# Kernel optimization log

Measured on AMD Instinct MI355X. Metric: run time of the kernel, lower is better.

Reference implementation:

```python
import jax, jax.numpy as jnp
import numpy as np

EPS = 1e-5

def _ln_stats(x):
    mu = jnp.mean(x, axis=-1, keepdims=True)
    var = jnp.mean((x - mu) ** 2, axis=-1, keepdims=True)
    return (x - mu) * jax.lax.rsqrt(var + EPS)

def setup_inputs() -> dict:
    B, S, H, I, E = 2, 2048, 1024, 4096, 8
    key = jax.random.key(0)
    ks = jax.random.split(key, 8)
    inp = {
        "hidden_states": jax.random.normal(ks[0], (B, S, H), dtype=jnp.float32),
        "router_ln_w": jnp.ones((H,), jnp.float32),
        "router_ln_b": jnp.zeros((H,), jnp.float32),
        "router_w": jax.random.normal(ks[1], (H, E), dtype=jnp.float32) * 0.02,
        "router_b": jnp.zeros((E,), jnp.float32),
        "exp_ln_w": jnp.ones((E, H), jnp.float32),
        "exp_ln_b": jnp.zeros((E, H), jnp.float32),
        "w1": jax.random.normal(ks[2], (E, H, I), dtype=jnp.float32) * 0.02,
        "b1": jnp.zeros((E, I), jnp.float32),
        "w2": jax.random.normal(ks[3], (E, I, H), dtype=jnp.float32) * 0.02,
        "b2": jnp.zeros((E, H), jnp.float32),
        "out_ln_w": jnp.ones((H,), jnp.float32),
        "out_ln_b": jnp.zeros((H,), jnp.float32),
    }
    return inp

def reference(hidden_states, router_ln_w, router_ln_b, router_w, router_b,
              exp_ln_w, exp_ln_b, w1, b1, w2, b2, out_ln_w, out_ln_b):
    K = 2  # experts_per_token
    x = hidden_states  # [B,S,H]
    xhat = _ln_stats(x)  # normalized (pre-affine) stats shared across LNs on x

    # Router: LayerNorm -> Linear -> top-k -> softmax over the k logits
    router_logits = (xhat * router_ln_w + router_ln_b) @ router_w + router_b  # [B,S,E]
    routing_weights, selected = jax.lax.top_k(router_logits, K)  # [B,S,K]
    routing_weights = jax.nn.softmax(routing_weights, axis=-1)

    # Dense per-expert pass over ALL tokens (faithful to the original),
    # dropout is identity in eval mode.
    xn = xhat[None] * exp_ln_w[:, None, None, :] + exp_ln_b[:, None, None, :]  # [E,B,S,H]
    h = jnp.einsum('ebsh,ehi->ebsi', xn, w1) + b1[:, None, None, :]            # [E,B,S,I]
    h = jax.nn.gelu(h, approximate=False)
    eo = jnp.einsum('ebsi,eih->ebsh', h, w2) + b2[:, None, None, :]            # [E,B,S,H]

    # Masked combine == gather selected experts and weight-sum (top-k indices are distinct)
    eo = jnp.moveaxis(eo, 0, 2)  # [B,S,E,H]
    gathered = jnp.take_along_axis(eo, selected[..., None], axis=2)  # [B,S,K,H]
    combined = jnp.sum(routing_weights[..., None] * gathered, axis=2)  # [B,S,H]

    return _ln_stats(combined) * out_ln_w + out_ln_b
```

## Files before the change

kernel.cpp:

```cpp
#include <hip/hip_runtime.h>
#include <hip/hip_bf16.h>

#define T_TOK 4096
#define HDIM 1024
#define IDIM 4096
#define NEXP 8

typedef __bf16 bf16x8 __attribute__((ext_vector_type(8)));
typedef float f32x4 __attribute__((ext_vector_type(4)));
typedef unsigned short us8 __attribute__((ext_vector_type(8)));

__device__ __forceinline__ unsigned short f2bf(float f) {
    union { float f; unsigned int u; } v; v.f = f;
    unsigned int u = v.u;
    unsigned int r = u + 0x7fffu + ((u >> 16) & 1u);
    return (unsigned short)(r >> 16);
}
__device__ __forceinline__ float bf2f(unsigned short b) {
    union { unsigned int u; float f; } v; v.u = ((unsigned int)b) << 16;
    return v.f;
}

__device__ __forceinline__ void gll16(const unsigned short* g, unsigned short* lds) {
    __builtin_amdgcn_global_load_lds(
        (const __attribute__((address_space(1))) unsigned int*)g,
        (__attribute__((address_space(3))) unsigned int*)lds, 16, 0, 0);
}

__device__ __forceinline__ float gelu_f(float v) {
    float x = v * 0.70710678118654752f;
    float ax = fabsf(x);
    float t = __builtin_amdgcn_rcpf(1.0f + 0.3275911f * ax);
    float p = t * (0.254829592f + t * (-0.284496736f + t * (1.421413741f
              + t * (-1.453152027f + t * 1.061405429f))));
    float ex = __expf(-x * x);
    float er = 1.0f - p * ex;
    er = copysignf(er, x);
    return 0.5f * v * (1.0f + er);
}

__global__ __launch_bounds__(256) void k_cvt_t(const float* __restrict__ src,
                                               unsigned short* __restrict__ dst,
                                               int R, int C) {
    __shared__ unsigned short tl[64][72];
    const int e = blockIdx.z;
    const int c0 = blockIdx.x * 64, r0 = blockIdx.y * 64;
    const int tid = threadIdx.x;
    #pragma unroll
    for (int it = 0; it < 4; it++) {
        int idx = it * 256 + tid;
        int rl = idx >> 4, cl = (idx & 15) * 4;
        float4 v = *(const float4*)(src + ((size_t)e * R + r0 + rl) * C + c0 + cl);
        tl[cl + 0][rl] = f2bf(v.x);
        tl[cl + 1][rl] = f2bf(v.y);
        tl[cl + 2][rl] = f2bf(v.z);
        tl[cl + 3][rl] = f2bf(v.w);
    }
    __syncthreads();
    #pragma unroll
    for (int it = 0; it < 2; it++) {
        int idx = it * 256 + tid;
        int cl = idx >> 3, ch = idx & 7;
        us8 v;
        __builtin_memcpy(&v, &tl[cl][ch * 8], 16);
        *(us8*)(dst + ((size_t)e * C + c0 + cl) * R + r0 + ch * 8) = v;
    }
}

__global__ __launch_bounds__(256) void k_ln_router(
    const float* __restrict__ x, const float* __restrict__ rlw, const float* __restrict__ rlb,
    const float* __restrict__ rw, const float* __restrict__ rb,
    unsigned short* __restrict__ xhat, int* __restrict__ counts,
    int* __restrict__ ltok, float* __restrict__ lwt)
{
    const int t = blockIdx.x, tid = threadIdx.x;
    const float4 v = *(const float4*)(x + (size_t)t * HDIM + tid * 4);
    float s  = v.x + v.y + v.z + v.w;
    float sq = v.x*v.x + v.y*v.y + v.z*v.z + v.w*v.w;
    for (int o = 32; o > 0; o >>= 1) { s += __shfl_xor(s, o); sq += __shfl_xor(sq, o); }
    __shared__ float red[8];
    __shared__ float stats[2];
    const int wid = tid >> 6, lane = tid & 63;
    if (lane == 0) { red[wid] = s; red[4 + wid] = sq; }
    __syncthreads();
    if (tid == 0) {
        float S = red[0] + red[1] + red[2] + red[3];
        float Q = red[4] + red[5] + red[6] + red[7];
        float mu = S / (float)HDIM;
        float var = Q / (float)HDIM - mu * mu;
        stats[0] = mu; stats[1] = rsqrtf(var + 1e-5f);
    }
    __syncthreads();
    const float mu = stats[0], rstd = stats[1];
    float xh[4];
    xh[0] = (v.x - mu) * rstd; xh[1] = (v.y - mu) * rstd;
    xh[2] = (v.z - mu) * rstd; xh[3] = (v.w - mu) * rstd;
    ushort4 o4;
    o4.x = f2bf(xh[0]); o4.y = f2bf(xh[1]); o4.z = f2bf(xh[2]); o4.w = f2bf(xh[3]);
    *(ushort4*)(xhat + (size_t)t * HDIM + tid * 4) = o4;

    float p[8];
    #pragma unroll
    for (int e = 0; e < 8; e++) p[e] = 0.f;
    const float4 w4 = *(const float4*)(rlw + tid * 4);
    const float4 b4 = *(const float4*)(rlb + tid * 4);
    const float wl[4] = { w4.x, w4.y, w4.z, w4.w };
    const float bl[4] = { b4.x, b4.y, b4.z, b4.w };
    #pragma unroll
    for (int j = 0; j < 4; j++) {
        float rl = xh[j] * wl[j] + bl[j];
        const float* wr = rw + (size_t)(tid * 4 + j) * 8;
        float4 wa = *(const float4*)(wr);
        float4 wb = *(const float4*)(wr + 4);
        p[0] += rl * wa.x; p[1] += rl * wa.y; p[2] += rl * wa.z; p[3] += rl * wa.w;
        p[4] += rl * wb.x; p[5] += rl * wb.y; p[6] += rl * wb.z; p[7] += rl * wb.w;
    }
    #pragma unroll
    for (int e = 0; e < 8; e++)
        for (int o = 32; o > 0; o >>= 1) p[e] += __shfl_xor(p[e], o);
    __shared__ float pw[4][8];
    if (lane == 0) {
        #pragma unroll
        for (int e = 0; e < 8; e++) pw[wid][e] = p[e];
    }
    __syncthreads();
    if (tid == 0) {
        float lg[8];
        #pragma unroll
        for (int e = 0; e < 8; e++)
            lg[e] = pw[0][e] + pw[1][e] + pw[2][e] + pw[3][e] + rb[e];
        int i0 = 0;
        #pragma unroll
        for (int e = 1; e < 8; e++) if (lg[e] > lg[i0]) i0 = e;
        int i1 = (i0 == 0) ? 1 : 0;
        #pragma unroll
        for (int e = 0; e < 8; e++) if (e != i0 && lg[e] > lg[i1]) i1 = e;
        float e1 = expf(lg[i1] - lg[i0]);
        float w0 = 1.f / (1.f + e1);
        float w1 = 1.f - w0;
        int p0 = atomicAdd(&counts[i0], 1);
        ltok[i0 * T_TOK + p0] = t * 2 + 0; lwt[i0 * T_TOK + p0] = w0;
        int p1 = atomicAdd(&counts[i1], 1);
        ltok[i1 * T_TOK + p1] = t * 2 + 1; lwt[i1 * T_TOK + p1] = w1;
    }
}

__global__ void k_offs(const int* __restrict__ counts, int* __restrict__ offs) {
    if (threadIdx.x == 0 && blockIdx.x == 0) {
        int a = 0;
        for (int e = 0; e < NEXP; e++) { offs[e] = a; a += counts[e]; }
        offs[NEXP] = a;
    }
}

__global__ __launch_bounds__(256) void k_ag_build(
    const unsigned short* __restrict__ xhat, const float* __restrict__ elw, const float* __restrict__ elb,
    const int* __restrict__ counts, const int* __restrict__ offs, const int* __restrict__ ltok,
    unsigned short* __restrict__ ag)
{
    const int e = blockIdx.z, rt = blockIdx.x, cc = blockIdx.y;
    const int ne = counts[e];
    if (rt * 128 >= ne) return;
    const int off = offs[e];
    const int tid = threadIdx.x;
    const int row = rt * 128 + (tid >> 1);
    if (row >= ne) return;
    const int tok = ltok[e * T_TOK + row] >> 1;
    const int cb = cc * 256 + (tid & 1) * 128;
    const unsigned short* src = xhat + (size_t)tok * HDIM + cb;
    unsigned short* dst = ag + (size_t)(off + row) * HDIM + cb;
    const float* wv = elw + (size_t)e * HDIM + cb;
    const float* bv = elb + (size_t)e * HDIM + cb;
    #pragma unroll
    for (int j = 0; j < 128; j += 8) {
        us8 xv = *(const us8*)(src + j);
        us8 o;
        #pragma unroll
        for (int q = 0; q < 8; q++)
            o[q] = f2bf(bf2f(xv[q]) * wv[j + q] + bv[j + q]);
        *(us8*)(dst + j) = o;
    }
}


#define GEMM_STAGE(gA, gB, ldst, ko, KSTRIDE)                                   \
    {                                                                           \
        _Pragma("unroll")                                                       \
        for (int i_ = 0; i_ < 4; i_++) {                                        \
            gll16(gA + (size_t)(8 * i_) * KSTRIDE + (ko), ldst##A + i_ * 512);  \
            gll16(gB + (size_t)(8 * i_) * KSTRIDE + (ko), ldst##B + i_ * 512);  \
        }                                                                       \
    }

#define GEMM_COMPUTE(ASb, BSb)                                                  \
    {                                                                           \
        _Pragma("unroll")                                                       \
        for (int ks_ = 0; ks_ < 64; ks_ += 32) {                                \
            const int ch_ = ks_ >> 3;                                           \
            bf16x8 af[4], bfr[4];                                               \
            _Pragma("unroll")                                                   \
            for (int i_ = 0; i_ < 4; i_++)                                      \
                __builtin_memcpy(&af[i_],                                       \
                    (ASb) + (wm + i_ * 16 + fr) * 64                            \
                          + (((quad + ch_) ^ (fr & 7)) * 8), 16);               \
            _Pragma("unroll")                                                   \
            for (int j_ = 0; j_ < 4; j_++)                                      \
                __builtin_memcpy(&bfr[j_],                                      \
                    (BSb) + (wn + j_ * 16 + fr) * 64                            \
                          + (((quad + ch_) ^ (fr & 7)) * 8), 16);               \
            _Pragma("unroll")                                                   \
            for (int i_ = 0; i_ < 4; i_++)                                      \
                _Pragma("unroll")                                               \
                for (int j_ = 0; j_ < 4; j_++)                                  \
                    acc[i_][j_] = __builtin_amdgcn_mfma_f32_16x16x32_bf16(      \
                        af[i_], bfr[j_], acc[i_][j_], 0, 0, 0);                 \
        }                                                                       \
    }

__global__ __launch_bounds__(256) void k_gemm1(
    const unsigned short* __restrict__ ag, const unsigned short* __restrict__ wbf,
    const float* __restrict__ b1,
    const int* __restrict__ counts, const int* __restrict__ offs,
    unsigned short* __restrict__ hbuf)
{
    const int ct = blockIdx.x, rt = blockIdx.y, e = blockIdx.z;
    const int ne = counts[e];
    if (rt * 128 >= ne) return;
    const int off = offs[e];
    __shared__ unsigned short As[2][128 * 64];
    __shared__ unsigned short Bs[2][128 * 64];
    const int tid = threadIdx.x, wid = tid >> 6, lane = tid & 63;
    const int lrow = lane >> 3, lchunk = (lane ^ lrow) & 7;

    const unsigned short* gA = ag + (size_t)(off + rt * 128 + 32 * wid + lrow) * HDIM + lchunk * 8;
    const unsigned short* gB = wbf + (size_t)e * IDIM * HDIM
                             + (size_t)(ct * 128 + 32 * wid + lrow) * HDIM + lchunk * 8;

    f32x4 acc[4][4];
    #pragma unroll
    for (int i = 0; i < 4; i++)
        #pragma unroll
        for (int j = 0; j < 4; j++) acc[i][j] = (f32x4){0.f, 0.f, 0.f, 0.f};

    const int wm = (wid & 1) * 64, wn = (wid >> 1) * 64;
    const int fr = lane & 15, quad = lane >> 4;

    unsigned short* l0A = &As[0][wid * 2048];
    unsigned short* l0B = &Bs[0][wid * 2048];
    unsigned short* l1A = &As[1][wid * 2048];
    unsigned short* l1B = &Bs[1][wid * 2048];

    const int NK = HDIM / 64;
    GEMM_STAGE(gA, gB, l0, 0, HDIM);
    #pragma unroll 1
    for (int kt = 0; kt < NK - 1; ++kt) {
        const int b = kt & 1;
        if (b == 0) { GEMM_STAGE(gA, gB, l1, (kt + 1) * 64, HDIM); }
        else        { GEMM_STAGE(gA, gB, l0, (kt + 1) * 64, HDIM); }
        asm volatile("s_waitcnt vmcnt(8)" ::: "memory");
        asm volatile("s_barrier" ::: "memory");
        GEMM_COMPUTE(&As[b][0], &Bs[b][0]);
        asm volatile("s_barrier" ::: "memory");
    }
    asm volatile("s_waitcnt vmcnt(0)" ::: "memory");
    asm volatile("s_barrier" ::: "memory");
    GEMM_COMPUTE(&As[(NK - 1) & 1][0], &Bs[(NK - 1) & 1][0]);

    float bias[4];
    #pragma unroll
    for (int j = 0; j < 4; j++) bias[j] = b1[e * IDIM + ct * 128 + wn + j * 16 + fr];
    #pragma unroll
    for (int i = 0; i < 4; i++) {
        #pragma unroll
        for (int rg = 0; rg < 4; rg++) {
            const int r = rt * 128 + wm + i * 16 + quad * 4 + rg;
            if (r < ne) {
                unsigned short* hrow = hbuf + (size_t)(off + r) * IDIM + ct * 128 + wn + fr;
                #pragma unroll
                for (int j = 0; j < 4; j++)
                    hrow[j * 16] = f2bf(gelu_f(acc[i][j][rg] + bias[j]));
            }
        }
    }
}

__global__ __launch_bounds__(256) void k_gemm2(
    const unsigned short* __restrict__ hbuf, const unsigned short* __restrict__ wbf,
    const float* __restrict__ b2,
    const int* __restrict__ counts, const int* __restrict__ offs,
    const int* __restrict__ ltok, const float* __restrict__ lwt,
    float* __restrict__ eo)
{
    const int ct = blockIdx.x, rt = blockIdx.y, e = blockIdx.z;
    const int ne = counts[e];
    if (rt * 128 >= ne) return;
    const int off = offs[e];
    __shared__ unsigned short As[2][128 * 64];
    __shared__ unsigned short Bs[2][128 * 64];
    const int tid = threadIdx.x, wid = tid >> 6, lane = tid & 63;
    const int lrow = lane >> 3, lchunk = (lane ^ lrow) & 7;

    const unsigned short* gA = hbuf + (size_t)(off + rt * 128 + 32 * wid + lrow) * IDIM + lchunk * 8;
    const unsigned short* gB = wbf + (size_t)e * HDIM * IDIM
                             + (size_t)(ct * 128 + 32 * wid + lrow) * IDIM + lchunk * 8;

    f32x4 acc[4][4];
    #pragma unroll
    for (int i = 0; i < 4; i++)
        #pragma unroll
        for (int j = 0; j < 4; j++) acc[i][j] = (f32x4){0.f, 0.f, 0.f, 0.f};

    const int wm = (wid & 1) * 64, wn = (wid >> 1) * 64;
    const int fr = lane & 15, quad = lane >> 4;

    unsigned short* l0A = &As[0][wid * 2048];
    unsigned short* l0B = &Bs[0][wid * 2048];
    unsigned short* l1A = &As[1][wid * 2048];
    unsigned short* l1B = &Bs[1][wid * 2048];

    const int NK = IDIM / 64;
    GEMM_STAGE(gA, gB, l0, 0, IDIM);
    #pragma unroll 1
    for (int kt = 0; kt < NK - 1; ++kt) {
        const int b = kt & 1;
        if (b == 0) { GEMM_STAGE(gA, gB, l1, (kt + 1) * 64, IDIM); }
        else        { GEMM_STAGE(gA, gB, l0, (kt + 1) * 64, IDIM); }
        asm volatile("s_waitcnt vmcnt(8)" ::: "memory");
        asm volatile("s_barrier" ::: "memory");
        GEMM_COMPUTE(&As[b][0], &Bs[b][0]);
        asm volatile("s_barrier" ::: "memory");
    }
    asm volatile("s_waitcnt vmcnt(0)" ::: "memory");
    asm volatile("s_barrier" ::: "memory");
    GEMM_COMPUTE(&As[(NK - 1) & 1][0], &Bs[(NK - 1) & 1][0]);

    float bias[4];
    #pragma unroll
    for (int j = 0; j < 4; j++) bias[j] = b2[e * HDIM + ct * 128 + wn + j * 16 + fr];
    #pragma unroll
    for (int i = 0; i < 4; i++) {
        #pragma unroll
        for (int rg = 0; rg < 4; rg++) {
            const int r = rt * 128 + wm + i * 16 + quad * 4 + rg;
            if (r < ne) {
                const int d = ltok[e * T_TOK + r];
                const float w = lwt[e * T_TOK + r];
                float* erow = eo + (size_t)d * HDIM + ct * 128 + wn + fr;
                #pragma unroll
                for (int j = 0; j < 4; j++)
                    erow[j * 16] = (acc[i][j][rg] + bias[j]) * w;
            }
        }
    }
}

__global__ __launch_bounds__(256) void k_final(
    const float* __restrict__ eo, const float* __restrict__ ow, const float* __restrict__ ob,
    float* __restrict__ out)
{
    const int t = blockIdx.x, tid = threadIdx.x;
    const float4 a = *(const float4*)(eo + (size_t)(t * 2 + 0) * HDIM + tid * 4);
    const float4 b = *(const float4*)(eo + (size_t)(t * 2 + 1) * HDIM + tid * 4);
    float c0 = a.x + b.x, c1 = a.y + b.y, c2 = a.z + b.z, c3 = a.w + b.w;
    float s = c0 + c1 + c2 + c3;
    float sq = c0*c0 + c1*c1 + c2*c2 + c3*c3;
    for (int o = 32; o > 0; o >>= 1) { s += __shfl_xor(s, o); sq += __shfl_xor(sq, o); }
    __shared__ float red[8];
    __shared__ float stats[2];
    const int wid = tid >> 6, lane = tid & 63;
    if (lane == 0) { red[wid] = s; red[4 + wid] = sq; }
    __syncthreads();
    if (tid == 0) {
        float S = red[0] + red[1] + red[2] + red[3];
        float Q = red[4] + red[5] + red[6] + red[7];
        float mu = S / (float)HDIM;
        float var = Q / (float)HDIM - mu * mu;
        stats[0] = mu; stats[1] = rsqrtf(var + 1e-5f);
    }
    __syncthreads();
    const float mu = stats[0], rstd = stats[1];
    const float4 w4 = *(const float4*)(ow + tid * 4);
    const float4 b4 = *(const float4*)(ob + tid * 4);
    float4 o;
    o.x = (c0 - mu) * rstd * w4.x + b4.x;
    o.y = (c1 - mu) * rstd * w4.y + b4.y;
    o.z = (c2 - mu) * rstd * w4.z + b4.z;
    o.w = (c3 - mu) * rstd * w4.w + b4.w;
    *(float4*)(out + (size_t)t * HDIM + tid * 4) = o;
}

extern "C" void kernel_launch(void* const* d_in, const int* in_sizes, int n_in,
                              void* d_out, int out_size, void* d_ws, size_t ws_size,
                              hipStream_t stream) {
    const float* x   = (const float*)d_in[0];
    const float* rlw = (const float*)d_in[1];
    const float* rlb = (const float*)d_in[2];
    const float* rw  = (const float*)d_in[3];
    const float* rb  = (const float*)d_in[4];
    const float* elw = (const float*)d_in[5];
    const float* elb = (const float*)d_in[6];
    const float* w1  = (const float*)d_in[7];
    const float* b1  = (const float*)d_in[8];
    const float* w2  = (const float*)d_in[9];
    const float* b2  = (const float*)d_in[10];
    const float* ow  = (const float*)d_in[11];
    const float* ob  = (const float*)d_in[12];
    float* out = (float*)d_out;

    char* ws = (char*)d_ws;
    const size_t MB = 1024 * 1024;
    unsigned short* wbf  = (unsigned short*)(ws);
    unsigned short* hbuf = (unsigned short*)(ws + 64 * MB);
    unsigned short* xhat = (unsigned short*)(ws + 64 * MB);
    unsigned short* ag   = (unsigned short*)(ws + 128 * MB);
    float* eo            = (float*)(ws + 128 * MB);
    char* tail           = ws + 160 * MB;
    int* ltok            = (int*)(tail);
    float* lwt           = (float*)(tail + 131072);
    int* counts          = (int*)(tail + 262144);
    int* offs            = (int*)(tail + 262144 + 64);

    hipMemsetAsync(counts, 0, 8 * sizeof(int), stream);
    k_cvt_t<<<dim3(IDIM / 64, HDIM / 64, NEXP), dim3(256), 0, stream>>>(w1, wbf, HDIM, IDIM);
    k_ln_router<<<dim3(T_TOK), dim3(256), 0, stream>>>(x, rlw, rlb, rw, rb, xhat, counts, ltok, lwt);
    k_offs<<<dim3(1), dim3(64), 0, stream>>>(counts, offs);
    k_ag_build<<<dim3(32, 4, NEXP), dim3(256), 0, stream>>>(xhat, elw, elb, counts, offs, ltok, ag);
    k_gemm1<<<dim3(32, 32, NEXP), dim3(256), 0, stream>>>(ag, wbf, b1, counts, offs, hbuf);
    k_cvt_t<<<dim3(HDIM / 64, IDIM / 64, NEXP), dim3(256), 0, stream>>>(w2, wbf, IDIM, HDIM);
    k_gemm2<<<dim3(8, 32, NEXP), dim3(256), 0, stream>>>(hbuf, wbf, b2, counts, offs, ltok, lwt, eo);
    k_final<<<dim3(T_TOK), dim3(256), 0, stream>>>(eo, ow, ob, out);
}
```

Measured before the change: 727.9 us.

## Halve GEMM K-tile, compact row-block schedule, and separate w2 conversion buffer

The grouped GEMMs now use a K-step of 32 instead of 64, which halves shared memory per block, and declare launch bounds of 5 blocks per SM to raise occupancy. A new scheduling kernel builds a compact list of (expert, row-tile) pairs so the grid no longer launches the many empty blocks that the old 3D grid created for underfilled experts. When the workspace is large enough, w2 is converted into its own buffer ahead of time instead of after gemm1. The cost is twice as many barrier and sync iterations per K, and a fixed cap of 72 row-blocks.

```diff
diff --git a/kernel.cpp b/kernel.cpp
--- a/kernel.cpp
+++ b/kernel.cpp
@@ -5,6 +5,7 @@
 #define HDIM 1024
 #define IDIM 4096
 #define NEXP 8
+#define MAXRB 72
 
 typedef __bf16 bf16x8 __attribute__((ext_vector_type(8)));
 typedef float f32x4 __attribute__((ext_vector_type(4)));
@@ -145,11 +146,18 @@
     }
 }
 
-__global__ void k_offs(const int* __restrict__ counts, int* __restrict__ offs) {
+__global__ void k_sched(const int* __restrict__ counts, int* __restrict__ offs,
+                        int* __restrict__ rb_e, int* __restrict__ rb_rt) {
     if (threadIdx.x == 0 && blockIdx.x == 0) {
         int a = 0;
         for (int e = 0; e < NEXP; e++) { offs[e] = a; a += counts[e]; }
         offs[NEXP] = a;
+        int i = 0;
+        for (int e = 0; e < NEXP; e++) {
+            int nrb = (counts[e] + 127) >> 7;
+            for (int rt = 0; rt < nrb; rt++) { rb_e[i] = e; rb_rt[i] = rt; i++; }
+        }
+        for (; i < MAXRB; i++) { rb_e[i] = -1; rb_rt[i] = 0; }
     }
 }
 
@@ -183,58 +191,44 @@
 }
 
 
-#define GEMM_STAGE(gA, gB, ldst, ko, KSTRIDE)                                   \
+#define GEMM_COMPUTE32(ASb, BSb)                                                \
     {                                                                           \
+        bf16x8 af[4], bfr[4];                                                   \
+        const int sw_ = (quad ^ ((fr >> 1) & 3)) * 8;                           \
         _Pragma("unroll")                                                       \
-        for (int i_ = 0; i_ < 4; i_++) {                                        \
-            gll16(gA + (size_t)(8 * i_) * KSTRIDE + (ko), ldst##A + i_ * 512);  \
-            gll16(gB + (size_t)(8 * i_) * KSTRIDE + (ko), ldst##B + i_ * 512);  \
-        }                                                                       \
-    }
-
-#define GEMM_COMPUTE(ASb, BSb)                                                  \
-    {                                                                           \
+        for (int i_ = 0; i_ < 4; i_++)                                          \
+            __builtin_memcpy(&af[i_], (ASb) + (wm + i_ * 16 + fr) * 32 + sw_, 16);\
         _Pragma("unroll")                                                       \
-        for (int ks_ = 0; ks_ < 64; ks_ += 32) {                                \
-            const int ch_ = ks_ >> 3;                                           \
-            bf16x8 af[4], bfr[4];                                               \
-            _Pragma("unroll")                                                   \
-            for (int i_ = 0; i_ < 4; i_++)                                      \
-                __builtin_memcpy(&af[i_],                                       \
-                    (ASb) + (wm + i_ * 16 + fr) * 64                            \
-                          + (((quad + ch_) ^ (fr & 7)) * 8), 16);               \
+        for (int j_ = 0; j_ < 4; j_++)                                          \
+            __builtin_memcpy(&bfr[j_], (BSb) + (wn + j_ * 16 + fr) * 32 + sw_, 16);\
+        _Pragma("unroll")                                                       \
+        for (int i_ = 0; i_ < 4; i_++)                                          \
             _Pragma("unroll")                                                   \
             for (int j_ = 0; j_ < 4; j_++)                                      \
-                __builtin_memcpy(&bfr[j_],                                      \
-                    (BSb) + (wn + j_ * 16 + fr) * 64                            \
-                          + (((quad + ch_) ^ (fr & 7)) * 8), 16);               \
-            _Pragma("unroll")                                                   \
-            for (int i_ = 0; i_ < 4; i_++)                                      \
-                _Pragma("unroll")                                               \
-                for (int j_ = 0; j_ < 4; j_++)                                  \
-                    acc[i_][j_] = __builtin_amdgcn_mfma_f32_16x16x32_bf16(      \
-                        af[i_], bfr[j_], acc[i_][j_], 0, 0, 0);                 \
-        }                                                                       \
-    }
-
-__global__ __launch_bounds__(256) void k_gemm1(
+                acc[i_][j_] = __builtin_amdgcn_mfma_f32_16x16x32_bf16(          \
+                    af[i_], bfr[j_], acc[i_][j_], 0, 0, 0);                     \
+    }
+
+__global__ __launch_bounds__(256, 5) void k_gemm1(
     const unsigned short* __restrict__ ag, const unsigned short* __restrict__ wbf,
     const float* __restrict__ b1,
     const int* __restrict__ counts, const int* __restrict__ offs,
+    const int* __restrict__ rb_e, const int* __restrict__ rb_rt,
     unsigned short* __restrict__ hbuf)
 {
-    const int ct = blockIdx.x, rt = blockIdx.y, e = blockIdx.z;
-    const int ne = counts[e];
-    if (rt * 128 >= ne) return;
-    const int off = offs[e];
-    __shared__ unsigned short As[2][128 * 64];
-    __shared__ unsigned short Bs[2][128 * 64];
+    const int e = rb_e[blockIdx.y];
+    if (e < 0) return;
+    const int rt = rb_rt[blockIdx.y], ct = blockIdx.x;
+    const int ne = counts[e], off = offs[e];
+    __shared__ unsigned short As[2 * 128 * 32];
+    __shared__ unsigned short Bs[2 * 128 * 32];
     const int tid = threadIdx.x, wid = tid >> 6, lane = tid & 63;
-    const int lrow = lane >> 3, lchunk = (lane ^ lrow) & 7;
-
-    const unsigned short* gA = ag + (size_t)(off + rt * 128 + 32 * wid + lrow) * HDIM + lchunk * 8;
+    const int srow = 32 * wid + (lane >> 2);
+    const int kswz = ((lane & 3) ^ ((lane >> 3) & 3)) * 8;
+    const unsigned short* gA = ag + (size_t)(off + rt * 128 + srow) * HDIM + kswz;
     const unsigned short* gB = wbf + (size_t)e * IDIM * HDIM
-                             + (size_t)(ct * 128 + 32 * wid + lrow) * HDIM + lchunk * 8;
+                             + (size_t)(ct * 128 + srow) * HDIM + kswz;
+    const int wso = wid * 1024;
 
     f32x4 acc[4][4];
     #pragma unroll
@@ -245,26 +239,29 @@
     const int wm = (wid & 1) * 64, wn = (wid >> 1) * 64;
     const int fr = lane & 15, quad = lane >> 4;
 
-    unsigned short* l0A = &As[0][wid * 2048];
-    unsigned short* l0B = &Bs[0][wid * 2048];
-    unsigned short* l1A = &As[1][wid * 2048];
-    unsigned short* l1B = &Bs[1][wid * 2048];
-
-    const int NK = HDIM / 64;
-    GEMM_STAGE(gA, gB, l0, 0, HDIM);
+    const int NK = HDIM / 32;
+    {
+        unsigned short* dA = As + wso;
+        unsigned short* dB = Bs + wso;
+        gll16(gA, dA); gll16(gA + (size_t)16 * HDIM, dA + 512);
+        gll16(gB, dB); gll16(gB + (size_t)16 * HDIM, dB + 512);
+    }
     #pragma unroll 1
     for (int kt = 0; kt < NK - 1; ++kt) {
         const int b = kt & 1;
-        if (b == 0) { GEMM_STAGE(gA, gB, l1, (kt + 1) * 64, HDIM); }
-        else        { GEMM_STAGE(gA, gB, l0, (kt + 1) * 64, HDIM); }
-        asm volatile("s_waitcnt vmcnt(8)" ::: "memory");
+        unsigned short* dA = As + (1 - b) * 4096 + wso;
+        unsigned short* dB = Bs + (1 - b) * 4096 + wso;
+        const size_t ko = (size_t)(kt + 1) * 32;
+        gll16(gA + ko, dA); gll16(gA + (size_t)16 * HDIM + ko, dA + 512);
+        gll16(gB + ko, dB); gll16(gB + (size_t)16 * HDIM + ko, dB + 512);
+        asm volatile("s_waitcnt vmcnt(4)" ::: "memory");
         asm volatile("s_barrier" ::: "memory");
-        GEMM_COMPUTE(&As[b][0], &Bs[b][0]);
+        GEMM_COMPUTE32(As + b * 4096, Bs + b * 4096);
         asm volatile("s_barrier" ::: "memory");
     }
     asm volatile("s_waitcnt vmcnt(0)" ::: "memory");
     asm volatile("s_barrier" ::: "memory");
-    GEMM_COMPUTE(&As[(NK - 1) & 1][0], &Bs[(NK - 1) & 1][0]);
+    GEMM_COMPUTE32(As + ((NK - 1) & 1) * 4096, Bs + ((NK - 1) & 1) * 4096);
 
     float bias[4];
     #pragma unroll
@@ -284,25 +281,27 @@
     }
 }
 
-__global__ __launch_bounds__(256) void k_gemm2(
+__global__ __launch_bounds__(256, 5) void k_gemm2(
     const unsigned short* __restrict__ hbuf, const unsigned short* __restrict__ wbf,
     const float* __restrict__ b2,
     const int* __restrict__ counts, const int* __restrict__ offs,
+    const int* __restrict__ rb_e, const int* __restrict__ rb_rt,
     const int* __restrict__ ltok, const float* __restrict__ lwt,
     float* __restrict__ eo)
 {
-    const int ct = blockIdx.x, rt = blockIdx.y, e = blockIdx.z;
-    const int ne = counts[e];
-    if (rt * 128 >= ne) return;
-    const int off = offs[e];
-    __shared__ unsigned short As[2][128 * 64];
-    __shared__ unsigned short Bs[2][128 * 64];
+    const int e = rb_e[blockIdx.y];
+    if (e < 0) return;
+    const int rt = rb_rt[blockIdx.y], ct = blockIdx.x;
+    const int ne = counts[e], off = offs[e];
+    __shared__ unsigned short As[2 * 128 * 32];
+    __shared__ unsigned short Bs[2 * 128 * 32];
     const int tid = threadIdx.x, wid = tid >> 6, lane = tid & 63;
-    const int lrow = lane >> 3, lchunk = (lane ^ lrow) & 7;
-
-    const unsigned short* gA = hbuf + (size_t)(off + rt * 128 + 32 * wid + lrow) * IDIM + lchunk * 8;
+    const int srow = 32 * wid + (lane >> 2);
+    const int kswz = ((lane & 3) ^ ((lane >> 3) & 3)) * 8;
+    const unsigned short* gA = hbuf + (size_t)(off + rt * 128 + srow) * IDIM + kswz;
     const unsigned short* gB = wbf + (size_t)e * HDIM * IDIM
-                             + (size_t)(ct * 128 + 32 * wid + lrow) * IDIM + lchunk * 8;
+                             + (size_t)(ct * 128 + srow) * IDIM + kswz;
+    const int wso = wid * 1024;
 
     f32x4 acc[4][4];
     #pragma unroll
@@ -313,26 +312,29 @@
     const int wm = (wid & 1) * 64, wn = (wid >> 1) * 64;
     const int fr = lane & 15, quad = lane >> 4;
 
-    unsigned short* l0A = &As[0][wid * 2048];
-    unsigned short* l0B = &Bs[0][wid * 2048];
-    unsigned short* l1A = &As[1][wid * 2048];
-    unsigned short* l1B = &Bs[1][wid * 2048];
-
-    const int NK = IDIM / 64;
-    GEMM_STAGE(gA, gB, l0, 0, IDIM);
+    const int NK = IDIM / 32;
+    {
+        unsigned short* dA = As + wso;
+        unsigned short* dB = Bs + wso;
+        gll16(gA, dA); gll16(gA + (size_t)16 * IDIM, dA + 512);
+        gll16(gB, dB); gll16(gB + (size_t)16 * IDIM, dB + 512);
+    }
     #pragma unroll 1
     for (int kt = 0; kt < NK - 1; ++kt) {
         const int b = kt & 1;
-        if (b == 0) { GEMM_STAGE(gA, gB, l1, (kt + 1) * 64, IDIM); }
-        else        { GEMM_STAGE(gA, gB, l0, (kt + 1) * 64, IDIM); }
-        asm volatile("s_waitcnt vmcnt(8)" ::: "memory");
+        unsigned short* dA = As + (1 - b) * 4096 + wso;
+        unsigned short* dB = Bs + (1 - b) * 4096 + wso;
+        const size_t ko = (size_t)(kt + 1) * 32;
+        gll16(gA + ko, dA); gll16(gA + (size_t)16 * IDIM + ko, dA + 512);
+        gll16(gB + ko, dB); gll16(gB + (size_t)16 * IDIM + ko, dB + 512);
+        asm volatile("s_waitcnt vmcnt(4)" ::: "memory");
         asm volatile("s_barrier" ::: "memory");
-        GEMM_COMPUTE(&As[b][0], &Bs[b][0]);
+        GEMM_COMPUTE32(As + b * 4096, Bs + b * 4096);
         asm volatile("s_barrier" ::: "memory");
     }
     asm volatile("s_waitcnt vmcnt(0)" ::: "memory");
     asm volatile("s_barrier" ::: "memory");
-    GEMM_COMPUTE(&As[(NK - 1) & 1][0], &Bs[(NK - 1) & 1][0]);
+    GEMM_COMPUTE32(As + ((NK - 1) & 1) * 4096, Bs + ((NK - 1) & 1) * 4096);
 
     float bias[4];
     #pragma unroll
@@ -407,26 +409,36 @@
     const float* ob  = (const float*)d_in[12];
     float* out = (float*)d_out;
 
+    const size_t MB = 1024 * 1024;
     char* ws = (char*)d_ws;
-    const size_t MB = 1024 * 1024;
-    unsigned short* wbf  = (unsigned short*)(ws);
+    const bool big = ws_size >= 242 * MB;
+    unsigned short* wbf1 = (unsigned short*)(ws);
     unsigned short* hbuf = (unsigned short*)(ws + 64 * MB);
     unsigned short* xhat = (unsigned short*)(ws + 64 * MB);
-    unsigned short* ag   = (unsigned short*)(ws + 128 * MB);
-    float* eo            = (float*)(ws + 128 * MB);
-    char* tail           = ws + 160 * MB;
+    unsigned short* wbf2 = big ? (unsigned short*)(ws + 128 * MB) : wbf1;
+    float* eo            = big ? (float*)(ws + 192 * MB) : (float*)(ws + 128 * MB);
+    unsigned short* ag   = big ? (unsigned short*)(ws + 224 * MB)
+                               : (unsigned short*)(ws + 128 * MB);
+    char* tail           = ws + (big ? 241 * MB : 160 * MB);
     int* ltok            = (int*)(tail);
     float* lwt           = (float*)(tail + 131072);
     int* counts          = (int*)(tail + 262144);
     int* offs            = (int*)(tail + 262144 + 64);
+    int* rb_e            = (int*)(tail + 262144 + 128);
+    int* rb_rt           = (int*)(tail + 262144 + 512);
 
     hipMemsetAsync(counts, 0, 8 * sizeof(int), stream);
-    k_cvt_t<<<dim3(IDIM / 64, HDIM / 64, NEXP), dim3(256), 0, stream>>>(w1, wbf, HDIM, IDIM);
+    k_cvt_t<<<dim3(IDIM / 64, HDIM / 64, NEXP), dim3(256), 0, stream>>>(w1, wbf1, HDIM, IDIM);
+    if (big)
+        k_cvt_t<<<dim3(HDIM / 64, IDIM / 64, NEXP), dim3(256), 0, stream>>>(w2, wbf2, IDIM, HDIM);
     k_ln_router<<<dim3(T_TOK), dim3(256), 0, stream>>>(x, rlw, rlb, rw, rb, xhat, counts, ltok, lwt);
-    k_offs<<<dim3(1), dim3(64), 0, stream>>>(counts, offs);
+    k_sched<<<dim3(1), dim3(64), 0, stream>>>(counts, offs, rb_e, rb_rt);
     k_ag_build<<<dim3(32, 4, NEXP), dim3(256), 0, stream>>>(xhat, elw, elb, counts, offs, ltok, ag);
-    k_gemm1<<<dim3(32, 32, NEXP), dim3(256), 0, stream>>>(ag, wbf, b1, counts, offs, hbuf);
-    k_cvt_t<<<dim3(HDIM / 64, IDIM / 64, NEXP), dim3(256), 0, stream>>>(w2, wbf, IDIM, HDIM);
-    k_gemm2<<<dim3(8, 32, NEXP), dim3(256), 0, stream>>>(hbuf, wbf, b2, counts, offs, ltok, lwt, eo);
+    k_gemm1<<<dim3(IDIM / 128, MAXRB), dim3(256), 0, stream>>>(
+        ag, wbf1, b1, counts, offs, rb_e, rb_rt, hbuf);
+    if (!big)
+        k_cvt_t<<<dim3(HDIM / 64, IDIM / 64, NEXP), dim3(256), 0, stream>>>(w2, wbf2, IDIM, HDIM);
+    k_gemm2<<<dim3(HDIM / 128, MAXRB), dim3(256), 0, stream>>>(
+        hbuf, wbf2, b2, counts, offs, rb_e, rb_rt, ltok, lwt, eo);
     k_final<<<dim3(T_TOK), dim3(256), 0, stream>>>(eo, ow, ob, out);
 }
```

After: 715.0 us. No clear change (-1.8%).
